# Optimization experiments

Hardware: AMD Instinct MI355X
Metric: run time of the kernel (lower is better)

Reference implementation:

```python
import jax, jax.numpy as jnp
import numpy as np

S, N, H = 4096, 32, 512

def setup_inputs() -> dict:
    key = jax.random.key(0)
    ks = jax.random.split(key, 8)
    scale = 1.0 / np.sqrt(H)
    return {
        "hidden": jax.random.normal(ks[0], (N, H), dtype=jnp.float32),
        "encoder_outputs": jax.random.normal(ks[1], (S, N, H), dtype=jnp.float32),
        "W_w": jax.random.uniform(ks[2], (H, H), jnp.float32, -scale, scale),
        "W_b": jax.random.uniform(ks[3], (H,), jnp.float32, -scale, scale),
        "U_w": jax.random.uniform(ks[4], (H, H), jnp.float32, -scale, scale),
        "U_b": jax.random.uniform(ks[5], (H,), jnp.float32, -scale, scale),
        "v_w": jax.random.uniform(ks[6], (1, H), jnp.float32, -scale, scale),
        "v_b": jax.random.uniform(ks[7], (1,), jnp.float32, -scale, scale),
    }

def reference(hidden, encoder_outputs, W_w, W_b, U_w, U_b, v_w, v_b):
    # W(hidden): [N,H] -> broadcast over seq dim (equivalent to expand then Linear)
    wh = hidden @ W_w.T + W_b                      # [N, H]
    ue = jnp.einsum('snh,kh->snk', encoder_outputs, U_w) + U_b  # [S, N, H]
    energy = jnp.tanh(wh[None, :, :] + ue)         # [S, N, H]
    score = jnp.einsum('snh,oh->sno', energy, v_w) + v_b        # [S, N, 1]
    attention_weights = jax.nn.softmax(score, axis=0)           # softmax over seq
    context = jnp.sum(attention_weights * encoder_outputs, axis=0)  # [N, H]
    return (context, attention_weights)
```

## Files before the change

### kernel.cpp

```cpp
#include <hip/hip_runtime.h>
#include <hip/hip_bf16.h>

#define Sdim 4096
#define Ndim 32
#define Hdim 512
#define Mdim (Sdim * Ndim)

#define BM 128
#define BN 256
#define BK 64

#define SC 256
#define SCR (Sdim / SC)

typedef __bf16 bf16x8 __attribute__((ext_vector_type(8)));
typedef float f32x4 __attribute__((ext_vector_type(4)));
typedef unsigned short ushort8v __attribute__((ext_vector_type(8)));

__device__ __forceinline__ void load_lds16(const void* g, void* l) {
    __builtin_amdgcn_global_load_lds(
        (const __attribute__((address_space(1))) void*)g,
        (__attribute__((address_space(3))) void*)l, 16, 0, 0);
}

__device__ __forceinline__ float ftanh(float x) {
    float e = __expf(2.f * x);
    return 1.f - 2.f / (e + 1.f);
}

__global__ __launch_bounds__(256) void k_prep(
    const float* __restrict__ hidden, const float* __restrict__ Ww,
    const float* __restrict__ Wb, const float* __restrict__ Ubias,
    float* __restrict__ bias, const float* __restrict__ Uw,
    unsigned short* __restrict__ Ub16) {
    const int t = threadIdx.x;
    if (blockIdx.x < 128) {
        const int w = t >> 6, lane = t & 63;
        const int cc = blockIdx.x * 4 + w;
        const float4 w0 = *(const float4*)(Ww + (size_t)cc * Hdim + lane * 8);
        const float4 w1 =
            *(const float4*)(Ww + (size_t)cc * Hdim + lane * 8 + 4);
        const float wb = Wb[cc] + Ubias[cc];
        for (int n = 0; n < Ndim; ++n) {
            const float4 h0 = *(const float4*)(hidden + n * Hdim + lane * 8);
            const float4 h1 =
                *(const float4*)(hidden + n * Hdim + lane * 8 + 4);
            float p = w0.x * h0.x + w0.y * h0.y + w0.z * h0.z + w0.w * h0.w +
                      w1.x * h1.x + w1.y * h1.y + w1.z * h1.z + w1.w * h1.w;
            p += __shfl_xor(p, 1);  p += __shfl_xor(p, 2);
            p += __shfl_xor(p, 4);  p += __shfl_xor(p, 8);
            p += __shfl_xor(p, 16); p += __shfl_xor(p, 32);
            if (lane == 0) bias[n * Hdim + cc] = p + wb;
        }
    } else {
        const int i = (blockIdx.x - 128) * 256 + t;
        float4 v = ((const float4*)Uw)[i];
        union { __hip_bfloat162 h[2]; ushort4 u; } r;
        r.h[0] = __float22bfloat162_rn(make_float2(v.x, v.y));
        r.h[1] = __float22bfloat162_rn(make_float2(v.z, v.w));
        ((ushort4*)Ub16)[i] = r.u;
    }
}

__global__ __launch_bounds__(512, 4) void k_gemm_score(
    const float* __restrict__ enc,
    const unsigned short* __restrict__ Ub,
    const float* __restrict__ bias,
    const float* __restrict__ vw,
    float* __restrict__ scorep) {
    __shared__ __align__(16) unsigned short Asm[BM][72];
    __shared__ __align__(16) unsigned short Bsm[BN * BK];
    __shared__ float ssm[4][BM];

    const int t = threadIdx.x;
    const int lane = t & 63;
    const int w = t >> 6;
    const int wM = w >> 2;
    const int wN = w & 3;
    const int c = lane & 15;
    const int q = lane >> 4;

    const int x = blockIdx.x;
    const int rowblk = (x & 7) | ((x >> 4) << 3);
    const int colblk = (x >> 3) & 1;
    const int mBase = rowblk * BM;
    const int colBase = colblk * BN;

    const int ar = t >> 2;
    const int aq = t & 3;
    const int asw = ((ar >> 3) & 1) << 1;
    const float4* arow =
        (const float4*)(enc + (size_t)(mBase + ar) * Hdim) + aq * 4;
    unsigned short* awr = &Asm[ar][((2 * aq) ^ asw) * 8];

    const int coff = lane >> 3;
    const int bch = (lane & 7) ^ coff;
    const unsigned short* bsrc =
        Ub + (size_t)(colBase + w * 8 + coff) * Hdim + bch * 8;
    unsigned short* bdst = Bsm + (w * 8) * BK;

    const int sA = ((c >> 3) & 1) << 1;
    const int sB = c & 7;

    f32x4 acc[4][4];
#pragma unroll
    for (int i = 0; i < 4; ++i)
#pragma unroll
        for (int j = 0; j < 4; ++j) acc[i][j] = (f32x4){0.f, 0.f, 0.f, 0.f};

    float4 a0 = *(const float4*)(arow + 0);
    float4 a1 = *(const float4*)(arow + 1);
    float4 a2 = *(const float4*)(arow + 2);
    float4 a3 = *(const float4*)(arow + 3);

#pragma unroll 1
    for (int kk = 0; kk < Hdim / BK; ++kk) {
        asm volatile("" ::: "memory");
        __builtin_amdgcn_s_barrier();
        asm volatile("" ::: "memory");
        __builtin_amdgcn_sched_barrier(0);

#pragma unroll
        for (int g = 0; g < 4; ++g)
            load_lds16(bsrc + (size_t)g * 64 * Hdim + kk * BK,
                       bdst + g * 64 * BK);
        asm volatile("" ::: "memory");
        __builtin_amdgcn_sched_barrier(0);

        union { __hip_bfloat162 h[4]; ushort8v v; } p0, p1;
        p0.h[0] = __float22bfloat162_rn(make_float2(a0.x, a0.y));
        p0.h[1] = __float22bfloat162_rn(make_float2(a0.z, a0.w));
        p0.h[2] = __float22bfloat162_rn(make_float2(a1.x, a1.y));
        p0.h[3] = __float22bfloat162_rn(make_float2(a1.z, a1.w));
        p1.h[0] = __float22bfloat162_rn(make_float2(a2.x, a2.y));
        p1.h[1] = __float22bfloat162_rn(make_float2(a2.z, a2.w));
        p1.h[2] = __float22bfloat162_rn(make_float2(a3.x, a3.y));
        p1.h[3] = __float22bfloat162_rn(make_float2(a3.z, a3.w));
        *(ushort8v*)awr = p0.v;
        *(ushort8v*)(awr + 8) = p1.v;

        const int kn = (kk < Hdim / BK - 1) ? kk + 1 : kk;
        const float4* ap = arow + kn * 16;
        a0 = ap[0]; a1 = ap[1]; a2 = ap[2]; a3 = ap[3];

        asm volatile("" ::: "memory");
        __builtin_amdgcn_sched_barrier(0);
        asm volatile("s_waitcnt vmcnt(4) lgkmcnt(0)" ::: "memory");
        __builtin_amdgcn_s_barrier();
        asm volatile("" ::: "memory");
        __builtin_amdgcn_sched_barrier(0);

#pragma unroll 1
        for (int h = 0; h < 2; ++h) {
            bf16x8 af[4], bfr[4];
#pragma unroll
            for (int mi = 0; mi < 4; ++mi) {
                const int row = wM * 64 + mi * 16 + c;
                af[mi] =
                    *(const bf16x8*)&Asm[row][(((h << 2) | q) ^ sA) * 8];
            }
#pragma unroll
            for (int ni = 0; ni < 4; ++ni) {
                const int lc = wN * 64 + ni * 16 + c;
                bfr[ni] = *(const bf16x8*)&Bsm[lc * BK +
                                               (((h << 2) | q) ^ sB) * 8];
            }
#pragma unroll
            for (int mi = 0; mi < 4; ++mi)
#pragma unroll
                for (int ni = 0; ni < 4; ++ni)
                    acc[mi][ni] = __builtin_amdgcn_mfma_f32_16x16x32_bf16(
                        af[mi], bfr[ni], acc[mi][ni], 0, 0, 0);
        }
    }
    asm volatile("" :: "v"(a0.x), "v"(a1.x), "v"(a2.x), "v"(a3.x));

    float vcol[4];
#pragma unroll
    for (int ni = 0; ni < 4; ++ni)
        vcol[ni] = vw[colBase + wN * 64 + ni * 16 + c];

#pragma unroll
    for (int mi = 0; mi < 4; ++mi) {
#pragma unroll
        for (int reg = 0; reg < 4; ++reg) {
            const int rl = wM * 64 + mi * 16 + q * 4 + reg;
            const int n = rl & 31;
            float p = 0.f;
#pragma unroll
            for (int ni = 0; ni < 4; ++ni) {
                const int col = colBase + wN * 64 + ni * 16 + c;
                float e = acc[mi][ni][reg] + bias[n * Hdim + col];
                p += vcol[ni] * ftanh(e);
            }
            p += __shfl_xor(p, 1);
            p += __shfl_xor(p, 2);
            p += __shfl_xor(p, 4);
            p += __shfl_xor(p, 8);
            if (c == 0) ssm[wN][rl] = p;
        }
    }
    __syncthreads();
    if (t < BM) {
        const int m = mBase + t;
        const float s = ssm[0][t] + ssm[1][t] + ssm[2][t] + ssm[3][t];
        scorep[colblk * Mdim + (m & 31) * Sdim + (m >> 5)] = s;
    }
}

__global__ __launch_bounds__(256) void k_sumexp(
    const float* __restrict__ scorep,
    float* __restrict__ sums) {
    const int n = blockIdx.x;
    const int t = threadIdx.x;
    const int w = t >> 6;
    const float4* p0 = (const float4*)(scorep + n * Sdim);
    const float4* p1 = (const float4*)(scorep + Mdim + n * Sdim);
    float s = 0.f;
    for (int i = t; i < Sdim / 4; i += 256) {
        const float4 a = p0[i], b = p1[i];
        s += __expf(a.x + b.x) + __expf(a.y + b.y) + __expf(a.z + b.z) +
             __expf(a.w + b.w);
    }
#pragma unroll
    for (int o = 32; o > 0; o >>= 1) s += __shfl_xor(s, o);
    __shared__ float red[4];
    if ((t & 63) == 0) red[w] = s;
    __syncthreads();
    if (t == 0) sums[n] = 1.f / (red[0] + red[1] + red[2] + red[3]);
}

__global__ __launch_bounds__(512) void k_context(
    const float* __restrict__ enc, const float* __restrict__ scorep,
    const float* __restrict__ sums, float* __restrict__ out_w,
    float* __restrict__ part) {
    const int sc = blockIdx.x;
    const int s0 = sc * SCR;
    const int t = threadIdx.x;

    __shared__ float wsm[SCR * Ndim];
    {
        const int sl = t >> 5, n = t & 31;
        const int s = s0 + sl;
        const float sv = scorep[n * Sdim + s] + scorep[Mdim + n * Sdim + s];
        const float wv = __expf(sv) * sums[n];
        wsm[t] = wv;
        out_w[(size_t)s * Ndim + n] = wv;
    }
    __syncthreads();

    float4 acc[8];
#pragma unroll
    for (int j = 0; j < 8; ++j) acc[j] = (float4){0.f, 0.f, 0.f, 0.f};

#pragma unroll 2
    for (int s = 0; s < SCR; ++s) {
        const float4* row =
            (const float4*)enc + (size_t)(s0 + s) * (Ndim * Hdim / 4);
#pragma unroll
        for (int j = 0; j < 8; ++j) {
            const int idx = t + j * 512;
            const float wv = wsm[s * 32 + (idx >> 7)];
            const float4 e = row[idx];
            acc[j].x += wv * e.x; acc[j].y += wv * e.y;
            acc[j].z += wv * e.z; acc[j].w += wv * e.w;
        }
    }
    float4* po = (float4*)part + (size_t)sc * 4096;
#pragma unroll
    for (int j = 0; j < 8; ++j) po[t + j * 512] = acc[j];
}

__global__ __launch_bounds__(256) void k_ctx_reduce(
    const float* __restrict__ part, float* __restrict__ out) {
    const int b = blockIdx.x;
    const int t = threadIdx.x;
    const int isub = t >> 6;
    const int jo = t & 63;
    const int j4 = b * 64 + jo;
    const float4* p = (const float4*)part;
    float4 s = {0.f, 0.f, 0.f, 0.f};
#pragma unroll 4
    for (int i = isub; i < SC; i += 4) {
        const float4 v = p[(size_t)i * 4096 + j4];
        s.x += v.x; s.y += v.y; s.z += v.z; s.w += v.w;
    }
    __shared__ __align__(16) float4 red[4][64];
    red[isub][jo] = s;
    __syncthreads();
    if (t < 64) {
        const float4 a = red[0][t], c = red[1][t], d = red[2][t],
                     e = red[3][t];
        float4 r;
        r.x = a.x + c.x + d.x + e.x;
        r.y = a.y + c.y + d.y + e.y;
        r.z = a.z + c.z + d.z + e.z;
        r.w = a.w + c.w + d.w + e.w;
        ((float4*)out)[b * 64 + t] = r;
    }
}

extern "C" void kernel_launch(void* const* d_in, const int* in_sizes, int n_in,
                              void* d_out, int out_size, void* d_ws,
                              size_t ws_size, hipStream_t stream) {
    const float* hidden = (const float*)d_in[0];
    const float* enc    = (const float*)d_in[1];
    const float* Ww     = (const float*)d_in[2];
    const float* Wb     = (const float*)d_in[3];
    const float* Uw     = (const float*)d_in[4];
    const float* Ubias  = (const float*)d_in[5];
    const float* vw     = (const float*)d_in[6];

    float* out = (float*)d_out;

    char* ws = (char*)d_ws;
    float* bias          = (float*)(ws);
    unsigned short* Ub16 = (unsigned short*)(ws + (64 << 10));
    float* scorep        = (float*)(ws + (576 << 10));
    float* sums          = (float*)(ws + (1600 << 10));
    float* part          = (float*)(ws + (1664 << 10));

    k_prep<<<384, 256, 0, stream>>>(hidden, Ww, Wb, Ubias, bias, Uw, Ub16);
    k_gemm_score<<<(Mdim / BM) * 2, 512, 0, stream>>>(enc, Ub16, bias, vw,
                                                      scorep);
    k_sumexp<<<Ndim, 256, 0, stream>>>(scorep, sums);
    k_context<<<SC, 512, 0, stream>>>(enc, scorep, sums, out + Ndim * Hdim,
                                      part);
    k_ctx_reduce<<<64, 256, 0, stream>>>(part, out);
}
```

Measured before the change: 487.5 us.

## Widen sum-exp and context kernels across more blocks using atomic partial sums

The softmax denominator kernel now runs 128 blocks instead of 32, one per quarter of each batch column. Each block atomically adds its partial exp-sum into a buffer that k_prep zeroes, and k_context divides by that sum instead of multiplying by a precomputed reciprocal. The context kernel doubles its sequence chunk count from 256 to 512 blocks, halving rows per block, to fill more compute units while streaming the encoder tensor. The cost is twice as many partial context vectors for the final reduction to read, plus float atomic ordering nondeterminism in the sums.

Result: no change. 496.9 us (+1.9%).

```diff
diff --git a/kernel.cpp b/kernel.cpp
--- a/kernel.cpp
+++ b/kernel.cpp
@@ -10,7 +10,7 @@
 #define BN 256
 #define BK 64
 
-#define SC 256
+#define SC 512
 #define SCR (Sdim / SC)
 
 typedef __bf16 bf16x8 __attribute__((ext_vector_type(8)));
@@ -32,9 +32,10 @@
     const float* __restrict__ hidden, const float* __restrict__ Ww,
     const float* __restrict__ Wb, const float* __restrict__ Ubias,
     float* __restrict__ bias, const float* __restrict__ Uw,
-    unsigned short* __restrict__ Ub16) {
+    unsigned short* __restrict__ Ub16, float* __restrict__ sums) {
     const int t = threadIdx.x;
     if (blockIdx.x < 128) {
+        if (blockIdx.x == 0 && t < Ndim) sums[t] = 0.f;
         const int w = t >> 6, lane = t & 63;
         const int cc = blockIdx.x * 4 + w;
         const float4 w0 = *(const float4*)(Ww + (size_t)cc * Hdim + lane * 8);
@@ -211,23 +212,20 @@
 __global__ __launch_bounds__(256) void k_sumexp(
     const float* __restrict__ scorep,
     float* __restrict__ sums) {
-    const int n = blockIdx.x;
-    const int t = threadIdx.x;
-    const int w = t >> 6;
-    const float4* p0 = (const float4*)(scorep + n * Sdim);
-    const float4* p1 = (const float4*)(scorep + Mdim + n * Sdim);
-    float s = 0.f;
-    for (int i = t; i < Sdim / 4; i += 256) {
-        const float4 a = p0[i], b = p1[i];
-        s += __expf(a.x + b.x) + __expf(a.y + b.y) + __expf(a.z + b.z) +
-             __expf(a.w + b.w);
-    }
+    const int b = blockIdx.x;
+    const int n = b >> 2;
+    const int i = (b & 3) * 256 + threadIdx.x;
+    const int t = threadIdx.x;
+    const float4 a = ((const float4*)(scorep + n * Sdim))[i];
+    const float4 c = ((const float4*)(scorep + Mdim + n * Sdim))[i];
+    float s = __expf(a.x + c.x) + __expf(a.y + c.y) + __expf(a.z + c.z) +
+              __expf(a.w + c.w);
 #pragma unroll
     for (int o = 32; o > 0; o >>= 1) s += __shfl_xor(s, o);
     __shared__ float red[4];
-    if ((t & 63) == 0) red[w] = s;
+    if ((t & 63) == 0) red[t >> 6] = s;
     __syncthreads();
-    if (t == 0) sums[n] = 1.f / (red[0] + red[1] + red[2] + red[3]);
+    if (t == 0) atomicAdd(&sums[n], red[0] + red[1] + red[2] + red[3]);
 }
 
 __global__ __launch_bounds__(512) void k_context(
@@ -239,11 +237,11 @@
     const int t = threadIdx.x;
 
     __shared__ float wsm[SCR * Ndim];
-    {
+    if (t < SCR * Ndim) {
         const int sl = t >> 5, n = t & 31;
         const int s = s0 + sl;
         const float sv = scorep[n * Sdim + s] + scorep[Mdim + n * Sdim + s];
-        const float wv = __expf(sv) * sums[n];
+        const float wv = __expf(sv) / sums[n];
         wsm[t] = wv;
         out_w[(size_t)s * Ndim + n] = wv;
     }
@@ -320,10 +318,11 @@
     float* sums          = (float*)(ws + (1600 << 10));
     float* part          = (float*)(ws + (1664 << 10));
 
-    k_prep<<<384, 256, 0, stream>>>(hidden, Ww, Wb, Ubias, bias, Uw, Ub16);
+    k_prep<<<384, 256, 0, stream>>>(hidden, Ww, Wb, Ubias, bias, Uw, Ub16,
+                                    sums);
     k_gemm_score<<<(Mdim / BM) * 2, 512, 0, stream>>>(enc, Ub16, bias, vw,
                                                       scorep);
-    k_sumexp<<<Ndim, 256, 0, stream>>>(scorep, sums);
+    k_sumexp<<<128, 256, 0, stream>>>(scorep, sums);
     k_context<<<SC, 512, 0, stream>>>(enc, scorep, sums, out + Ndim * Hdim,
                                       part);
     k_ctx_reduce<<<64, 256, 0, stream>>>(part, out);
```
